# Kernel tuning notes

Hardware: AMD Instinct MI355X
Metric: run time of the kernel (lower is better)

The kernel has to match this reference:

```python
import jax, jax.numpy as jnp
import numpy as np

EPS = 1e-10
BETA = 1.0


def setup_inputs() -> dict:
    key = jax.random.key(0)
    k1, k2 = jax.random.split(key)
    N, C = 2097152, 32
    logits = jax.random.normal(k1, (N, C), dtype=jnp.float32)
    labels = jax.random.randint(k2, (N,), 0, C, dtype=jnp.int64)
    unc_th = jnp.float32(1.0)
    return {"logits": logits, "labels": labels, "unc_th": unc_th}


def reference(logits, labels, unc_th):
    # probs: [N, C]
    probs = jax.nn.softmax(logits, axis=1)
    confidences = jnp.max(probs, axis=1)            # [N]
    predictions = jnp.argmax(probs, axis=1)         # [N]
    # predictive entropy (type=0 path): [N]
    unc = -jnp.sum(probs * jnp.log(probs + EPS), axis=-1)

    accurate = labels == predictions                 # [N] bool
    certain = unc <= unc_th                          # [N] bool
    t = jnp.tanh(unc)

    zero = jnp.zeros((), dtype=probs.dtype)
    n_ac = jnp.sum(jnp.where(accurate & certain, confidences * (1.0 - t), zero))
    n_au = jnp.sum(jnp.where(accurate & ~certain, confidences * t, zero))
    n_ic = jnp.sum(jnp.where(~accurate & certain, (1.0 - confidences) * (1.0 - t), zero))
    n_iu = jnp.sum(jnp.where(~accurate & ~certain, (1.0 - confidences) * t, zero))

    avu = (n_ac + n_iu) / (n_ac + n_au + n_ic + n_iu + EPS)
    avu_loss = -BETA * jnp.log(avu + EPS)
    return jnp.reshape(avu_loss, (1,))
```

## Files before the change

### kernel.cpp

```cpp
#include <hip/hip_runtime.h>
#include <math.h>


#define AVU_EPS 1e-10f

__global__ __launch_bounds__(256) void avu_main_kernel(
    const float* __restrict__ logits,
    const int* __restrict__ labels,
    const float* __restrict__ unc_th_p,
    double* __restrict__ sums,
    int N)
{
    const float unc_th = unc_th_p[0];

    float acc0 = 0.f, acc1 = 0.f, acc2 = 0.f, acc3 = 0.f;

    const int stride = gridDim.x * blockDim.x;
    for (int row = blockIdx.x * blockDim.x + threadIdx.x; row < N; row += stride) {
        const float4* rp = (const float4*)(logits + (size_t)row * 32);
        float4 v[8];
#pragma unroll
        for (int j = 0; j < 8; ++j) v[j] = rp[j];

        float m = v[0].x;
        int idx = 0;
#pragma unroll
        for (int j = 0; j < 8; ++j) {
            const float* f = (const float*)&v[j];
#pragma unroll
            for (int k = 0; k < 4; ++k) {
                const int i = j * 4 + k;
                const float x = f[k];
                if (x > m) { m = x; idx = i; }
            }
        }

        float S = 0.f, dot = 0.f;
#pragma unroll
        for (int j = 0; j < 8; ++j) {
            const float* f = (const float*)&v[j];
#pragma unroll
            for (int k = 0; k < 4; ++k) {
                const float d = f[k] - m;
                const float e = __expf(d);
                S += e;
                dot += e * d;
            }
        }

        const float rS   = 1.0f / S;
        const float conf = rS;
        const float unc  = __logf(S) - dot * rS;
        const float t    = tanhf(unc);

        const bool accurate = (labels[row] == idx);
        const bool certain  = (unc <= unc_th);

        const float a = accurate ? conf : (1.0f - conf);
        const float w = certain ? (1.0f - t) : t;
        const float val = a * w;

        acc0 += ( accurate &&  certain) ? val : 0.f;
        acc1 += ( accurate && !certain) ? val : 0.f;
        acc2 += (!accurate &&  certain) ? val : 0.f;
        acc3 += (!accurate && !certain) ? val : 0.f;
    }

#pragma unroll
    for (int off = 32; off > 0; off >>= 1) {
        acc0 += __shfl_down(acc0, off);
        acc1 += __shfl_down(acc1, off);
        acc2 += __shfl_down(acc2, off);
        acc3 += __shfl_down(acc3, off);
    }

    __shared__ float red[4][4];
    const int wave = threadIdx.x >> 6;
    const int lane = threadIdx.x & 63;
    if (lane == 0) {
        red[wave][0] = acc0;
        red[wave][1] = acc1;
        red[wave][2] = acc2;
        red[wave][3] = acc3;
    }
    __syncthreads();

    if (threadIdx.x == 0) {
        double s0 = 0.0, s1 = 0.0, s2 = 0.0, s3 = 0.0;
#pragma unroll
        for (int w = 0; w < 4; ++w) {
            s0 += (double)red[w][0];
            s1 += (double)red[w][1];
            s2 += (double)red[w][2];
            s3 += (double)red[w][3];
        }
        atomicAdd(&sums[0], s0);
        atomicAdd(&sums[1], s1);
        atomicAdd(&sums[2], s2);
        atomicAdd(&sums[3], s3);
    }
}

__global__ void avu_final_kernel(const double* __restrict__ sums,
                                 float* __restrict__ out)
{
    const double n_ac = sums[0];
    const double n_au = sums[1];
    const double n_ic = sums[2];
    const double n_iu = sums[3];
    const double avu = (n_ac + n_iu) / (n_ac + n_au + n_ic + n_iu + 1e-10);
    out[0] = (float)(-log(avu + 1e-10));
}

extern "C" void kernel_launch(void* const* d_in, const int* in_sizes, int n_in,
                              void* d_out, int out_size, void* d_ws, size_t ws_size,
                              hipStream_t stream)
{
    const float* logits   = (const float*)d_in[0];
    const int*   labels   = (const int*)d_in[1];
    const float* unc_th   = (const float*)d_in[2];
    float*       out      = (float*)d_out;
    double*      sums     = (double*)d_ws;

    const int N = in_sizes[1];

    hipMemsetAsync(d_ws, 0, 4 * sizeof(double), stream);

    avu_main_kernel<<<2048, 256, 0, stream>>>(logits, labels, unc_th, sums, N);
    avu_final_kernel<<<1, 1, 0, stream>>>(sums, out);
}
```

Measured before the change: 407.0 us.

## Split each row across 8 lanes for coalesced loads and drop atomics

Each row of 32 logits is now handled by 8 lanes, each reading one float4, so a wave reads 1 KB of contiguous memory per step instead of each thread striding across its own 128-byte row. The max, argmax and softmax sums are combined with xor shuffles. Each wave works on a contiguous chunk of rows and prefetches the next float4 one iteration ahead. Per-block partial sums go to a workspace and are reduced by a single-wave final kernel, which removes the memset and the double atomics. tanh is replaced by an exp-based formula. The cost is extra shuffles per row, and only one lane in eight does the final per-row maths.

```diff
diff --git a/kernel.cpp b/kernel.cpp
--- a/kernel.cpp
+++ b/kernel.cpp
@@ -2,130 +2,156 @@
 #include <math.h>
 
 
-#define AVU_EPS 1e-10f
-
-__global__ __launch_bounds__(256) void avu_main_kernel(
+__global__ __launch_bounds__(256) void avu_main(
     const float* __restrict__ logits,
     const int* __restrict__ labels,
     const float* __restrict__ unc_th_p,
-    double* __restrict__ sums,
+    float4* __restrict__ partials,
     int N)
 {
     const float unc_th = unc_th_p[0];
+    const float4* __restrict__ p4 = (const float4*)logits;
+
+    const int lane = threadIdx.x & 63;
+    const int wave = threadIdx.x >> 6;
+    const int sub  = lane & 7;
+    const int rgrp = lane >> 3;
+
+    const int wavesPerBlock = blockDim.x >> 6;
+    const int W  = blockIdx.x * wavesPerBlock + wave;
+    const int TW = gridDim.x * wavesPerBlock;
+
+    const int G   = (N + 7) >> 3;
+    const int gpw = (G + TW - 1) / TW;
+    const int g0  = W * gpw;
+
+    const int totalF4 = N * 8;
 
     float acc0 = 0.f, acc1 = 0.f, acc2 = 0.f, acc3 = 0.f;
 
-    const int stride = gridDim.x * blockDim.x;
-    for (int row = blockIdx.x * blockDim.x + threadIdx.x; row < N; row += stride) {
-        const float4* rp = (const float4*)(logits + (size_t)row * 32);
-        float4 v[8];
-#pragma unroll
-        for (int j = 0; j < 8; ++j) v[j] = rp[j];
+    float4 v = make_float4(0.f, 0.f, 0.f, 0.f);
+    if (g0 < G) {
+        const int f4 = g0 * 64 + lane;
+        if (f4 < totalF4) v = p4[f4];
+    }
 
-        float m = v[0].x;
-        int idx = 0;
-#pragma unroll
-        for (int j = 0; j < 8; ++j) {
-            const float* f = (const float*)&v[j];
-#pragma unroll
-            for (int k = 0; k < 4; ++k) {
-                const int i = j * 4 + k;
-                const float x = f[k];
-                if (x > m) { m = x; idx = i; }
-            }
+    for (int i = 0; i < gpw; ++i) {
+        const int g = g0 + i;
+        if (g >= G) break;
+
+        float4 vn = make_float4(0.f, 0.f, 0.f, 0.f);
+        if (i + 1 < gpw && g + 1 < G) {
+            const int f4 = (g + 1) * 64 + lane;
+            if (f4 < totalF4) vn = p4[f4];
         }
 
-        float S = 0.f, dot = 0.f;
+        const int row   = (g << 3) + rgrp;
+        const bool valid = (row < N);
+        const int lab = valid ? labels[row] : -1;
+
+        const int base = sub << 2;
+        float m = v.x; int mi = base;
+        if (v.y > m) { m = v.y; mi = base + 1; }
+        if (v.z > m) { m = v.z; mi = base + 2; }
+        if (v.w > m) { m = v.w; mi = base + 3; }
+
 #pragma unroll
-        for (int j = 0; j < 8; ++j) {
-            const float* f = (const float*)&v[j];
+        for (int mask = 1; mask <= 4; mask <<= 1) {
+            const float om = __shfl_xor(m, mask);
+            const int   oi = __shfl_xor(mi, mask);
+            if (om > m || (om == m && oi < mi)) { m = om; mi = oi; }
+        }
+
+        const float d0 = v.x - m, d1 = v.y - m, d2 = v.z - m, d3 = v.w - m;
+        const float e0 = __expf(d0), e1 = __expf(d1);
+        const float e2 = __expf(d2), e3 = __expf(d3);
+        float S   = (e0 + e1) + (e2 + e3);
+        float dot = (e0 * d0 + e1 * d1) + (e2 * d2 + e3 * d3);
 #pragma unroll
-            for (int k = 0; k < 4; ++k) {
-                const float d = f[k] - m;
-                const float e = __expf(d);
-                S += e;
-                dot += e * d;
-            }
+        for (int mask = 1; mask <= 4; mask <<= 1) {
+            S   += __shfl_xor(S, mask);
+            dot += __shfl_xor(dot, mask);
         }
 
         const float rS   = 1.0f / S;
         const float conf = rS;
         const float unc  = __logf(S) - dot * rS;
-        const float t    = tanhf(unc);
+        const float t = 1.0f - 2.0f / (__expf(2.0f * unc) + 1.0f);
 
-        const bool accurate = (labels[row] == idx);
+        const bool accurate = (lab == mi);
         const bool certain  = (unc <= unc_th);
 
         const float a = accurate ? conf : (1.0f - conf);
         const float w = certain ? (1.0f - t) : t;
-        const float val = a * w;
+        float val = a * w;
+        val = (sub == 0 && valid) ? val : 0.f;
 
         acc0 += ( accurate &&  certain) ? val : 0.f;
         acc1 += ( accurate && !certain) ? val : 0.f;
         acc2 += (!accurate &&  certain) ? val : 0.f;
         acc3 += (!accurate && !certain) ? val : 0.f;
+
+        v = vn;
     }
 
 #pragma unroll
-    for (int off = 32; off > 0; off >>= 1) {
-        acc0 += __shfl_down(acc0, off);
-        acc1 += __shfl_down(acc1, off);
-        acc2 += __shfl_down(acc2, off);
-        acc3 += __shfl_down(acc3, off);
+    for (int mask = 1; mask <= 32; mask <<= 1) {
+        acc0 += __shfl_xor(acc0, mask);
+        acc1 += __shfl_xor(acc1, mask);
+        acc2 += __shfl_xor(acc2, mask);
+        acc3 += __shfl_xor(acc3, mask);
     }
 
-    __shared__ float red[4][4];
-    const int wave = threadIdx.x >> 6;
-    const int lane = threadIdx.x & 63;
-    if (lane == 0) {
-        red[wave][0] = acc0;
-        red[wave][1] = acc1;
-        red[wave][2] = acc2;
-        red[wave][3] = acc3;
-    }
+    __shared__ float4 red[4];
+    if (lane == 0) red[wave] = make_float4(acc0, acc1, acc2, acc3);
     __syncthreads();
 
     if (threadIdx.x == 0) {
-        double s0 = 0.0, s1 = 0.0, s2 = 0.0, s3 = 0.0;
-#pragma unroll
-        for (int w = 0; w < 4; ++w) {
-            s0 += (double)red[w][0];
-            s1 += (double)red[w][1];
-            s2 += (double)red[w][2];
-            s3 += (double)red[w][3];
+        float4 r = red[0];
+        for (int w2 = 1; w2 < wavesPerBlock; ++w2) {
+            const float4 q = red[w2];
+            r.x += q.x; r.y += q.y; r.z += q.z; r.w += q.w;
         }
-        atomicAdd(&sums[0], s0);
-        atomicAdd(&sums[1], s1);
-        atomicAdd(&sums[2], s2);
-        atomicAdd(&sums[3], s3);
+        partials[blockIdx.x] = r;
     }
 }
 
-__global__ void avu_final_kernel(const double* __restrict__ sums,
-                                 float* __restrict__ out)
+__global__ __launch_bounds__(64) void avu_final(
+    const float4* __restrict__ partials, int nPart,
+    float* __restrict__ out)
 {
-    const double n_ac = sums[0];
-    const double n_au = sums[1];
-    const double n_ic = sums[2];
-    const double n_iu = sums[3];
-    const double avu = (n_ac + n_iu) / (n_ac + n_au + n_ic + n_iu + 1e-10);
-    out[0] = (float)(-log(avu + 1e-10));
+    double s0 = 0.0, s1 = 0.0, s2 = 0.0, s3 = 0.0;
+    for (int i = threadIdx.x; i < nPart; i += 64) {
+        const float4 p = partials[i];
+        s0 += (double)p.x; s1 += (double)p.y;
+        s2 += (double)p.z; s3 += (double)p.w;
+    }
+#pragma unroll
+    for (int mask = 1; mask <= 32; mask <<= 1) {
+        s0 += __shfl_xor(s0, mask);
+        s1 += __shfl_xor(s1, mask);
+        s2 += __shfl_xor(s2, mask);
+        s3 += __shfl_xor(s3, mask);
+    }
+    if (threadIdx.x == 0) {
+        const double avu = (s0 + s3) / (s0 + s1 + s2 + s3 + 1e-10);
+        out[0] = (float)(-log(avu + 1e-10));
+    }
 }
 
 extern "C" void kernel_launch(void* const* d_in, const int* in_sizes, int n_in,
                               void* d_out, int out_size, void* d_ws, size_t ws_size,
                               hipStream_t stream)
 {
-    const float* logits   = (const float*)d_in[0];
-    const int*   labels   = (const int*)d_in[1];
-    const float* unc_th   = (const float*)d_in[2];
-    float*       out      = (float*)d_out;
-    double*      sums     = (double*)d_ws;
+    const float* logits = (const float*)d_in[0];
+    const int*   labels = (const int*)d_in[1];
+    const float* unc_th = (const float*)d_in[2];
+    float*       out    = (float*)d_out;
+    float4*      parts  = (float4*)d_ws;
 
     const int N = in_sizes[1];
+    const int BLOCKS = 2048;
 
-    hipMemsetAsync(d_ws, 0, 4 * sizeof(double), stream);
-
-    avu_main_kernel<<<2048, 256, 0, stream>>>(logits, labels, unc_th, sums, N);
-    avu_final_kernel<<<1, 1, 0, stream>>>(sums, out);
+    avu_main<<<BLOCKS, 256, 0, stream>>>(logits, labels, unc_th, parts, N);
+    avu_final<<<1, 64, 0, stream>>>(parts, BLOCKS, out);
 }
```

New measurement: 376.8 us. 1.08x faster.
